# Optimization experiments

Measured on AMD Instinct MI355X. Metric: run time of the kernel, lower is better.

The kernel has to match this reference:

```python
import jax, jax.numpy as jnp
import numpy as np

B, S, DX = 64, 4096, 512
Q, DQ = 128, 512

def setup_inputs() -> dict:
    key = jax.random.key(0)
    k1, k2, k3, k4 = jax.random.split(key, 4)
    x = jax.random.normal(k1, (B, S, DX), dtype=jnp.float32)
    query_matrix = jax.random.normal(k2, (B, Q, DQ), dtype=jnp.float32)
    # learned params (random_normal init in the original layer)
    W = jax.random.normal(k3, (DQ, DX), dtype=jnp.float32)
    p = jax.random.normal(k4, (Q, 1), dtype=jnp.float32)
    return {"x": x, "query_matrix": query_matrix, "W": W, "p": p}

def reference(x, query_matrix, W, p):
    # per-sample loop in the original: transpose(q_i) @ p -> [Dq, 1]; stacked & squeezed -> [B, Dq]
    new_q = jnp.einsum('bqd,q->bd', query_matrix, p[:, 0])          # [B, Dq]
    first = new_q @ W                                               # [B, Dx]
    scores = jnp.einsum('bd,bsd->bs', first, x)                     # [B, S]
    alpha = jax.nn.softmax(scores, axis=-1)                         # softmax over keys
    context = jnp.einsum('bs,bsd->bd', alpha, x)                    # batch_dot -> [B, Dx]
    return context
```

## Files before the change

kernel.cpp:

```cpp
#include <hip/hip_runtime.h>
#include <math.h>

#define BB 64
#define SS 4096
#define DXX 512
#define QQ 128
#define DQQ 512
#define SPLITS 16
#define CHUNK (SS / SPLITS)
#define NWAVES 4
#define ROWS_PER_WAVE (CHUNK / NWAVES)

__global__ __launch_bounds__(512) void compute_first(
        const float* __restrict__ qm, const float* __restrict__ W,
        const float* __restrict__ p, float* __restrict__ first) {
    int b = blockIdx.x;
    int t = threadIdx.x;
    __shared__ float sp[QQ];
    __shared__ float snq[DQQ];
    if (t < QQ) sp[t] = p[t];
    __syncthreads();

    const float* qb = qm + (size_t)b * QQ * DQQ + t;
    float acc = 0.f;
    #pragma unroll 8
    for (int q = 0; q < QQ; ++q) acc = fmaf(qb[(size_t)q * DQQ], sp[q], acc);
    snq[t] = acc;
    __syncthreads();

    float f = 0.f;
    #pragma unroll 8
    for (int dq = 0; dq < DQQ; ++dq) f = fmaf(snq[dq], W[(size_t)dq * DXX + t], f);
    first[b * DXX + t] = f;
}

__global__ __launch_bounds__(256) void attn_partial(
        const float* __restrict__ x, const float* __restrict__ first,
        float* __restrict__ pm, float* __restrict__ pl,
        float* __restrict__ pacc) {
    int blk  = blockIdx.x;
    int b    = blk / SPLITS;
    int sp   = blk % SPLITS;
    int tid  = threadIdx.x;
    int wave = tid >> 6;
    int lane = tid & 63;

    const float* fb = first + b * DXX;
    const float4 f0 = *(const float4*)(fb + lane * 4);
    const float4 f1 = *(const float4*)(fb + 256 + lane * 4);

    float m = -1e30f, l = 0.f;
    float4 a0 = {0.f, 0.f, 0.f, 0.f};
    float4 a1 = {0.f, 0.f, 0.f, 0.f};

    const float* xb = x + (size_t)b * SS * DXX;
    const int s0 = sp * CHUNK + wave;

    #pragma unroll 2
    for (int i = 0; i < ROWS_PER_WAVE; ++i) {
        const int s = s0 + i * NWAVES;
        const float* xr = xb + (size_t)s * DXX;
        const float4 x0 = *(const float4*)(xr + lane * 4);
        const float4 x1 = *(const float4*)(xr + 256 + lane * 4);

        float d = f0.x * x0.x + f0.y * x0.y + f0.z * x0.z + f0.w * x0.w
                + f1.x * x1.x + f1.y * x1.y + f1.z * x1.z + f1.w * x1.w;
        #pragma unroll
        for (int off = 32; off > 0; off >>= 1) d += __shfl_xor(d, off, 64);

        const float nm    = fmaxf(m, d);
        const float alpha = __expf(m - nm);
        const float w     = __expf(d - nm);
        l = l * alpha + w;
        a0.x = fmaf(a0.x, alpha, w * x0.x);
        a0.y = fmaf(a0.y, alpha, w * x0.y);
        a0.z = fmaf(a0.z, alpha, w * x0.z);
        a0.w = fmaf(a0.w, alpha, w * x0.w);
        a1.x = fmaf(a1.x, alpha, w * x1.x);
        a1.y = fmaf(a1.y, alpha, w * x1.y);
        a1.z = fmaf(a1.z, alpha, w * x1.z);
        a1.w = fmaf(a1.w, alpha, w * x1.w);
        m = nm;
    }

    __shared__ float sm[NWAVES];
    __shared__ float sl[NWAVES];
    __shared__ float sacc[NWAVES][DXX];
    if (lane == 0) { sm[wave] = m; sl[wave] = l; }
    float* sa = sacc[wave];
    *(float4*)(sa + lane * 4)       = a0;
    *(float4*)(sa + 256 + lane * 4) = a1;
    __syncthreads();

    const float M  = fmaxf(fmaxf(sm[0], sm[1]), fmaxf(sm[2], sm[3]));
    const float e0 = __expf(sm[0] - M), e1 = __expf(sm[1] - M);
    const float e2 = __expf(sm[2] - M), e3 = __expf(sm[3] - M);
    if (tid == 0) {
        pm[blk] = M;
        pl[blk] = sl[0] * e0 + sl[1] * e1 + sl[2] * e2 + sl[3] * e3;
    }
    #pragma unroll
    for (int dx = tid; dx < DXX; dx += 256) {
        pacc[(size_t)blk * DXX + dx] =
            sacc[0][dx] * e0 + sacc[1][dx] * e1 + sacc[2][dx] * e2 + sacc[3][dx] * e3;
    }
}

__global__ __launch_bounds__(256) void attn_finalize(
        const float* __restrict__ pm, const float* __restrict__ pl,
        const float* __restrict__ pacc, float* __restrict__ out) {
    int b = blockIdx.x;
    int tid = threadIdx.x;

    __shared__ float e[SPLITS];
    __shared__ float invL;
    if (tid == 0) {
        float M = -1e30f;
        for (int i = 0; i < SPLITS; ++i) M = fmaxf(M, pm[b * SPLITS + i]);
        float L = 0.f;
        for (int i = 0; i < SPLITS; ++i) {
            float ei = __expf(pm[b * SPLITS + i] - M);
            e[i] = ei;
            L += pl[b * SPLITS + i] * ei;
        }
        invL = 1.f / L;
    }
    __syncthreads();

    #pragma unroll
    for (int dx = tid; dx < DXX; dx += 256) {
        float v = 0.f;
        for (int i = 0; i < SPLITS; ++i)
            v = fmaf(pacc[(size_t)(b * SPLITS + i) * DXX + dx], e[i], v);
        out[b * DXX + dx] = v * invL;
    }
}

extern "C" void kernel_launch(void* const* d_in, const int* in_sizes, int n_in,
                              void* d_out, int out_size, void* d_ws, size_t ws_size,
                              hipStream_t stream) {
    const float* x  = (const float*)d_in[0];
    const float* qm = (const float*)d_in[1];
    const float* W  = (const float*)d_in[2];
    const float* p  = (const float*)d_in[3];
    float* out = (float*)d_out;

    float* ws    = (float*)d_ws;
    float* first = ws;
    float* pm    = first + BB * DXX;
    float* pl    = pm + BB * SPLITS;
    float* pacc  = pl + BB * SPLITS;

    compute_first<<<BB, 512, 0, stream>>>(qm, W, p, first);
    attn_partial<<<BB * SPLITS, 256, 0, stream>>>(x, first, pm, pl, pacc);
    attn_finalize<<<BB, 256, 0, stream>>>(pm, pl, pacc, out);
}
```

Before: 726.6 us.

## Batch four rows per wave with nontemporal loads and branchy online softmax

```diff
diff --git a/kernel.cpp b/kernel.cpp
--- a/kernel.cpp
+++ b/kernel.cpp
@@ -6,10 +6,13 @@
 #define DXX 512
 #define QQ 128
 #define DQQ 512
-#define SPLITS 16
+#define SPLITS 32
 #define CHUNK (SS / SPLITS)
 #define NWAVES 4
 #define ROWS_PER_WAVE (CHUNK / NWAVES)
+#define RB 4
+
+typedef float v4 __attribute__((ext_vector_type(4)));
 
 __global__ __launch_bounds__(512) void compute_first(
         const float* __restrict__ qm, const float* __restrict__ W,
@@ -46,41 +49,47 @@
     int lane = tid & 63;
 
     const float* fb = first + b * DXX;
-    const float4 f0 = *(const float4*)(fb + lane * 4);
-    const float4 f1 = *(const float4*)(fb + 256 + lane * 4);
+    const v4 f0 = *(const v4*)(fb + lane * 4);
+    const v4 f1 = *(const v4*)(fb + 256 + lane * 4);
 
     float m = -1e30f, l = 0.f;
-    float4 a0 = {0.f, 0.f, 0.f, 0.f};
-    float4 a1 = {0.f, 0.f, 0.f, 0.f};
+    v4 a0 = {0.f, 0.f, 0.f, 0.f};
+    v4 a1 = {0.f, 0.f, 0.f, 0.f};
 
     const float* xb = x + (size_t)b * SS * DXX;
     const int s0 = sp * CHUNK + wave;
 
-    #pragma unroll 2
-    for (int i = 0; i < ROWS_PER_WAVE; ++i) {
-        const int s = s0 + i * NWAVES;
-        const float* xr = xb + (size_t)s * DXX;
-        const float4 x0 = *(const float4*)(xr + lane * 4);
-        const float4 x1 = *(const float4*)(xr + 256 + lane * 4);
-
-        float d = f0.x * x0.x + f0.y * x0.y + f0.z * x0.z + f0.w * x0.w
-                + f1.x * x1.x + f1.y * x1.y + f1.z * x1.z + f1.w * x1.w;
+    for (int i = 0; i < ROWS_PER_WAVE; i += RB) {
+        v4 x0[RB], x1[RB];
+        float d[RB];
         #pragma unroll
-        for (int off = 32; off > 0; off >>= 1) d += __shfl_xor(d, off, 64);
-
-        const float nm    = fmaxf(m, d);
-        const float alpha = __expf(m - nm);
-        const float w     = __expf(d - nm);
-        l = l * alpha + w;
-        a0.x = fmaf(a0.x, alpha, w * x0.x);
-        a0.y = fmaf(a0.y, alpha, w * x0.y);
-        a0.z = fmaf(a0.z, alpha, w * x0.z);
-        a0.w = fmaf(a0.w, alpha, w * x0.w);
-        a1.x = fmaf(a1.x, alpha, w * x1.x);
-        a1.y = fmaf(a1.y, alpha, w * x1.y);
-        a1.z = fmaf(a1.z, alpha, w * x1.z);
-        a1.w = fmaf(a1.w, alpha, w * x1.w);
-        m = nm;
+        for (int r = 0; r < RB; ++r) {
+            const float* xr = xb + (size_t)(s0 + (i + r) * NWAVES) * DXX;
+            x0[r] = __builtin_nontemporal_load((const v4*)(xr + lane * 4));
+            x1[r] = __builtin_nontemporal_load((const v4*)(xr + 256 + lane * 4));
+            v4 t4 = f0 * x0[r] + f1 * x1[r];
+            d[r] = t4.x + t4.y + t4.z + t4.w;
+        }
+        #pragma unroll
+        for (int off = 32; off > 0; off >>= 1) {
+            #pragma unroll
+            for (int r = 0; r < RB; ++r) d[r] += __shfl_xor(d[r], off, 64);
+        }
+        #pragma unroll
+        for (int r = 0; r < RB; ++r) {
+            if (d[r] > m) {
+                const float alpha = __expf(m - d[r]);
+                m = d[r];
+                l = fmaf(l, alpha, 1.f);
+                a0 = a0 * alpha + x0[r];
+                a1 = a1 * alpha + x1[r];
+            } else {
+                const float w = __expf(d[r] - m);
+                l += w;
+                a0 += x0[r] * w;
+                a1 += x1[r] * w;
+            }
+        }
     }
 
     __shared__ float sm[NWAVES];
@@ -88,8 +97,8 @@
     __shared__ float sacc[NWAVES][DXX];
     if (lane == 0) { sm[wave] = m; sl[wave] = l; }
     float* sa = sacc[wave];
-    *(float4*)(sa + lane * 4)       = a0;
-    *(float4*)(sa + 256 + lane * 4) = a1;
+    *(v4*)(sa + lane * 4)       = a0;
+    *(v4*)(sa + 256 + lane * 4) = a1;
     __syncthreads();
 
     const float M  = fmaxf(fmaxf(sm[0], sm[1]), fmaxf(sm[2], sm[3]));
```

New measurement: 703.3 us. 1.03x faster.
